# Performance work log

Measured on AMD Instinct MI355X. Metric: run time of the kernel, lower is better.

## Reference

```python
import jax, jax.numpy as jnp
import numpy as np

B, A, C = 524288, 4, 9  # C = input_size + 1 (first channel is the initial hidden state)


def setup_inputs() -> dict:
    key = jax.random.key(0)
    ks = jax.random.split(key, 7)
    s = 1.0  # nn.GRU/Linear init is uniform(-1,1) for hidden=1; normal is fine for a numeric baseline
    return {
        "inputs": jax.random.normal(ks[0], (B, A, C), dtype=jnp.float32),
        "w_ih": jax.random.normal(ks[1], (3, C - 1), dtype=jnp.float32) * s,
        "w_hh": jax.random.normal(ks[2], (3, 1), dtype=jnp.float32) * s,
        "b_ih": jax.random.normal(ks[3], (3,), dtype=jnp.float32) * s,
        "b_hh": jax.random.normal(ks[4], (3,), dtype=jnp.float32) * s,
        "w_out": jax.random.normal(ks[5], (1, 1), dtype=jnp.float32) * s,
        "b_out": jax.random.normal(ks[6], (1,), dtype=jnp.float32) * s,
    }


def reference(inputs, w_ih, w_hh, b_ih, b_hh, w_out, b_out):
    b, a, c = inputs.shape
    flat = inputs.reshape(b * a, c)
    h = flat[:, :1]          # [N,1] initial hidden state
    x = flat[:, 1:]          # [N,C-1] GRU input (single timestep)
    gi = x @ w_ih.T + b_ih   # [N,3] input gates (r,z,n order, PyTorch convention)
    gh = h @ w_hh.T + b_hh   # [N,3] hidden gates
    r = jax.nn.sigmoid(gi[:, 0:1] + gh[:, 0:1])
    z = jax.nn.sigmoid(gi[:, 1:2] + gh[:, 1:2])
    n = jnp.tanh(gi[:, 2:3] + r * gh[:, 2:3])
    h_new = (1.0 - z) * n + z * h            # [N,1]
    out = h_new * w_out[0, 0] + b_out[0]     # Linear(1,1)
    return out.reshape(b, a, 1)
```

## Files before the change

### kernel.cpp

```cpp
#include <hip/hip_runtime.h>

__global__ __launch_bounds__(256) void gru_cell_kernel(
    const float* __restrict__ in,
    const float* __restrict__ w_ih,
    const float* __restrict__ w_hh,
    const float* __restrict__ b_ih,
    const float* __restrict__ b_hh,
    const float* __restrict__ w_out,
    const float* __restrict__ b_out,
    float* __restrict__ out,
    int n_rows)
{
    const int tid = blockIdx.x * blockDim.x + threadIdx.x;
    const int row0 = tid * 4;
    if (row0 >= n_rows) return;

    float wih[3][8];
#pragma unroll
    for (int g = 0; g < 3; ++g)
#pragma unroll
        for (int c = 0; c < 8; ++c)
            wih[g][c] = w_ih[g * 8 + c];
    const float whh0 = w_hh[0], whh1 = w_hh[1], whh2 = w_hh[2];
    const float bi0 = b_ih[0], bi1 = b_ih[1], bi2 = b_ih[2];
    const float bh0 = b_hh[0], bh1 = b_hh[1], bh2 = b_hh[2];
    const float wo = w_out[0], bo = b_out[0];

    float4 v[9];
    const float4* src = reinterpret_cast<const float4*>(in + (size_t)row0 * 9);
#pragma unroll
    for (int i = 0; i < 9; ++i) v[i] = src[i];
    const float* f = reinterpret_cast<const float*>(v);

    float4 o;
    float* op = reinterpret_cast<float*>(&o);
#pragma unroll
    for (int r = 0; r < 4; ++r) {
        const float* row = f + r * 9;
        const float h = row[0];
        float gi0 = bi0, gi1 = bi1, gi2 = bi2;
#pragma unroll
        for (int c = 0; c < 8; ++c) {
            const float x = row[1 + c];
            gi0 = fmaf(x, wih[0][c], gi0);
            gi1 = fmaf(x, wih[1][c], gi1);
            gi2 = fmaf(x, wih[2][c], gi2);
        }
        const float gh0 = fmaf(h, whh0, bh0);
        const float gh1 = fmaf(h, whh1, bh1);
        const float gh2 = fmaf(h, whh2, bh2);

        const float rg = 1.0f / (1.0f + __expf(-(gi0 + gh0)));
        const float z  = 1.0f / (1.0f + __expf(-(gi1 + gh1)));
        const float nn = tanhf(fmaf(rg, gh2, gi2));
        const float hn = (1.0f - z) * nn + z * h;
        op[r] = fmaf(hn, wo, bo);
    }
    *reinterpret_cast<float4*>(out + row0) = o;
}

extern "C" void kernel_launch(void* const* d_in, const int* in_sizes, int n_in,
                              void* d_out, int out_size, void* d_ws, size_t ws_size,
                              hipStream_t stream) {
    (void)n_in; (void)d_ws; (void)ws_size;
    const float* in    = (const float*)d_in[0];
    const float* w_ih  = (const float*)d_in[1];
    const float* w_hh  = (const float*)d_in[2];
    const float* b_ih  = (const float*)d_in[3];
    const float* b_hh  = (const float*)d_in[4];
    const float* w_out = (const float*)d_in[5];
    const float* b_out = (const float*)d_in[6];
    float* out = (float*)d_out;

    const int n_rows = out_size;
    const int rows_per_thread = 4;
    const int block = 256;
    const int threads = (n_rows + rows_per_thread - 1) / rows_per_thread;
    const int grid = (threads + block - 1) / block;

    gru_cell_kernel<<<grid, block, 0, stream>>>(in, w_ih, w_hh, b_ih, b_hh,
                                                w_out, b_out, out, n_rows);
}
```

Baseline: 18.76 us.

## Process eight rows per thread, use exp-based tanh and nontemporal stores

Doubles rows per thread from four to eight, so each thread issues eighteen 16-byte loads and two output vector stores. The input loads are moved ahead of the weight loads. tanhf is replaced with an exp-based formula, and output stores become nontemporal. The aim is more memory-level parallelism per thread and a cheaper transcendental, at the cost of halving the thread count and raising register pressure. The grid calculation now truncates n_rows/8, so any remainder rows would be dropped; this is safe for the given size.

```diff
diff --git a/kernel.cpp b/kernel.cpp
--- a/kernel.cpp
+++ b/kernel.cpp
@@ -1,6 +1,13 @@
 #include <hip/hip_runtime.h>
 
-__global__ __launch_bounds__(256) void gru_cell_kernel(
+
+constexpr int BLOCK = 256;
+constexpr int RPT   = 8;
+constexpr int F4PT  = RPT * 9 / 4;
+
+typedef float nfloat4 __attribute__((ext_vector_type(4)));
+
+__global__ __launch_bounds__(BLOCK) void gru_cell_kernel(
     const float* __restrict__ in,
     const float* __restrict__ w_ih,
     const float* __restrict__ w_hh,
@@ -12,8 +19,13 @@
     int n_rows)
 {
     const int tid = blockIdx.x * blockDim.x + threadIdx.x;
-    const int row0 = tid * 4;
+    const int row0 = tid * RPT;
     if (row0 >= n_rows) return;
+
+    nfloat4 v[F4PT];
+    const nfloat4* src = reinterpret_cast<const nfloat4*>(in + (size_t)row0 * 9);
+#pragma unroll
+    for (int i = 0; i < F4PT; ++i) v[i] = src[i];
 
     float wih[3][8];
 #pragma unroll
@@ -26,16 +38,11 @@
     const float bh0 = b_hh[0], bh1 = b_hh[1], bh2 = b_hh[2];
     const float wo = w_out[0], bo = b_out[0];
 
-    float4 v[9];
-    const float4* src = reinterpret_cast<const float4*>(in + (size_t)row0 * 9);
+    const float* f = reinterpret_cast<const float*>(v);
+    nfloat4 o[2];
+    float* op = reinterpret_cast<float*>(o);
 #pragma unroll
-    for (int i = 0; i < 9; ++i) v[i] = src[i];
-    const float* f = reinterpret_cast<const float*>(v);
-
-    float4 o;
-    float* op = reinterpret_cast<float*>(&o);
-#pragma unroll
-    for (int r = 0; r < 4; ++r) {
+    for (int r = 0; r < RPT; ++r) {
         const float* row = f + r * 9;
         const float h = row[0];
         float gi0 = bi0, gi1 = bi1, gi2 = bi2;
@@ -52,17 +59,21 @@
 
         const float rg = 1.0f / (1.0f + __expf(-(gi0 + gh0)));
         const float z  = 1.0f / (1.0f + __expf(-(gi1 + gh1)));
-        const float nn = tanhf(fmaf(rg, gh2, gi2));
+        const float y  = fmaf(rg, gh2, gi2);
+        const float nn = 2.0f / (1.0f + __expf(-2.0f * y)) - 1.0f;
         const float hn = (1.0f - z) * nn + z * h;
         op[r] = fmaf(hn, wo, bo);
     }
-    *reinterpret_cast<float4*>(out + row0) = o;
+
+    nfloat4* dst = reinterpret_cast<nfloat4*>(out + row0);
+    __builtin_nontemporal_store(o[0], dst);
+    __builtin_nontemporal_store(o[1], dst + 1);
 }
 
 extern "C" void kernel_launch(void* const* d_in, const int* in_sizes, int n_in,
                               void* d_out, int out_size, void* d_ws, size_t ws_size,
                               hipStream_t stream) {
-    (void)n_in; (void)d_ws; (void)ws_size;
+    (void)n_in; (void)d_ws; (void)ws_size; (void)in_sizes;
     const float* in    = (const float*)d_in[0];
     const float* w_ih  = (const float*)d_in[1];
     const float* w_hh  = (const float*)d_in[2];
@@ -73,11 +84,9 @@
     float* out = (float*)d_out;
 
     const int n_rows = out_size;
-    const int rows_per_thread = 4;
-    const int block = 256;
-    const int threads = (n_rows + rows_per_thread - 1) / rows_per_thread;
-    const int grid = (threads + block - 1) / block;
+    const int threads = n_rows / RPT;
+    const int grid = (threads + BLOCK - 1) / BLOCK;
 
-    gru_cell_kernel<<<grid, block, 0, stream>>>(in, w_ih, w_hh, b_ih, b_hh,
+    gru_cell_kernel<<<grid, BLOCK, 0, stream>>>(in, w_ih, w_hh, b_ih, b_hh,
                                                 w_out, b_out, out, n_rows);
 }
```

Measured after the change: 21.92 us. 16.9% more time.
